# Kernel tuning notes

Measured on AMD Instinct MI355X. Metric: run time of the kernel, lower is better.

## Reference

```python
import jax, jax.numpy as jnp
import numpy as np

N_NODES = 100000
N_EDGES = 1600000
IN_CH = 128
HID = 128
NUM_CLASSES = 10
NUM_GRAPHS = 128
SLOPE = 0.01  # F.leaky_relu default negative_slope


def _lin_params(key, fan_in, fan_out):
    kw, kb = jax.random.split(key)
    bound = 1.0 / np.sqrt(fan_in)
    W = jax.random.uniform(kw, (fan_in, fan_out), jnp.float32, -bound, bound)
    b = jax.random.uniform(kb, (fan_out,), jnp.float32, -bound, bound)
    return W, b


def setup_inputs() -> dict:
    key = jax.random.key(0)
    ks = jax.random.split(key, 8)
    x = jax.random.normal(ks[0], (N_NODES, IN_CH), jnp.float32)
    edge_index = jax.random.randint(ks[1], (2, N_EDGES), 0, N_NODES, jnp.int64)
    batch = jnp.sort(jax.random.randint(ks[2], (N_NODES,), 0, NUM_GRAPHS, jnp.int64))
    W1, b1 = _lin_params(ks[3], IN_CH, HID)
    W2, b2 = _lin_params(ks[4], HID, HID)
    W3, b3 = _lin_params(ks[5], HID, HID // 2)
    W4, b4 = _lin_params(ks[6], HID // 2, HID // 2)
    W5, b5 = _lin_params(ks[7], HID // 2, NUM_CLASSES)
    return {"x": x, "edge_index": edge_index, "batch": batch,
            "W1": W1, "b1": b1, "W2": W2, "b2": b2,
            "W3": W3, "b3": b3, "W4": W4, "b4": b4, "W5": W5, "b5": b5}


def gcn_conv(x, src, dst, W, b):
    # PyG GCNConv: h = x W; add self-loops; symmetric norm D^-1/2 (A+I) D^-1/2
    h = x @ W  # [N, F]
    n = x.shape[0]
    deg = jnp.zeros((n,), h.dtype).at[dst].add(1.0) + 1.0  # includes self-loop
    dinv = jax.lax.rsqrt(deg)
    norm = dinv[src] * dinv[dst]  # [E]
    agg = jnp.zeros_like(h).at[dst].add(h[src] * norm[:, None])
    agg = agg + h * (dinv * dinv)[:, None]  # self-loop term: 1/deg
    return agg + b


def reference(x, edge_index, batch, W1, b1, W2, b2, W3, b3, W4, b4, W5, b5):
    src, dst = edge_index[0], edge_index[1]
    h = jax.nn.leaky_relu(gcn_conv(x, src, dst, W1, b1), SLOPE)
    h = jax.nn.leaky_relu(gcn_conv(h, src, dst, W2, b2), SLOPE)
    # global mean pool over graphs
    sums = jax.ops.segment_sum(h, batch, num_segments=NUM_GRAPHS)
    cnts = jax.ops.segment_sum(jnp.ones((h.shape[0],), h.dtype), batch,
                               num_segments=NUM_GRAPHS)
    g = sums / jnp.maximum(cnts, 1.0)[:, None]  # [NUM_GRAPHS, HID]
    g = jax.nn.leaky_relu(g @ W3 + b3, SLOPE)
    g = jax.nn.leaky_relu(g @ W4 + b4, SLOPE)
    return g @ W5 + b5
```

## Files before the change

### kernel.cpp

```cpp
#include <hip/hip_runtime.h>
#include <hip/hip_bf16.h>


#define SLOPE 0.01f

__device__ __forceinline__ float lrelu(float x) { return x > 0.f ? x : SLOPE * x; }

__device__ __forceinline__ unsigned short f2bf(float f) {
    union { float f; unsigned u; } v; v.f = f;
    unsigned r = v.u + 0x7fffu + ((v.u >> 16) & 1u);
    return (unsigned short)(r >> 16);
}
__device__ __forceinline__ float bf_lo(unsigned x) {
    union { unsigned u; float f; } v; v.u = x << 16; return v.f;
}
__device__ __forceinline__ float bf_hi(unsigned x) {
    union { unsigned u; float f; } v; v.u = x & 0xffff0000u; return v.f;
}
__device__ __forceinline__ unsigned packbf(float lo, float hi) {
    return (unsigned)f2bf(lo) | ((unsigned)f2bf(hi) << 16);
}

typedef __attribute__((ext_vector_type(8))) short bf16x8;
typedef __attribute__((ext_vector_type(4))) float f32x4;
typedef __attribute__((ext_vector_type(2))) float f32x2;

#define LDA 136
#define CAPP 5120
#define MAXBUCK 400

__global__ void k_init(int* __restrict__ zbase, int nz,
                       const float* __restrict__ W1, unsigned short* __restrict__ WT1,
                       const float* __restrict__ W2, unsigned short* __restrict__ WT2,
                       const int* __restrict__ batch, int* __restrict__ gstart,
                       int N, int NG) {
    int b = blockIdx.x;
    if (b < 64) {
        int idx = b * 256 + threadIdx.x;
        int k = idx >> 7, n = idx & 127;
        WT1[n * 128 + k] = f2bf(W1[idx]);
    } else if (b < 128) {
        int idx = (b - 64) * 256 + threadIdx.x;
        int k = idx >> 7, n = idx & 127;
        WT2[n * 128 + k] = f2bf(W2[idx]);
    } else if (b == 128) {
        int g = threadIdx.x;
        if (g <= NG) {
            int lo = 0, hi = N;
            while (lo < hi) { int mid = (lo + hi) >> 1; if (batch[mid] < g) lo = mid + 1; else hi = mid; }
            gstart[g] = lo;
        }
    } else {
        int i = (b - 129) * 256 + threadIdx.x;
        if (i < nz) zbase[i] = 0;
    }
}

template<bool IN_BF16, bool SCALE>
__device__ __forceinline__ void gemm_body(const void* __restrict__ Xv,
                                          const unsigned short* __restrict__ WT,
                                          unsigned short* __restrict__ Y, int M,
                                          unsigned short* Bs, int bid,
                                          const float* __restrict__ dinvg) {
    int t = threadIdx.x;
    int row0 = bid * 64;
    int w = t >> 6, l = t & 63;
    int lr = l & 15;
    int ko = (l >> 4) * 8;

    int gr = row0 + w * 16 + lr;
    bool inb = gr < M;
    bf16x8 afr[4];
    if (IN_BF16) {
        const unsigned short* Xrow = (const unsigned short*)Xv + (size_t)gr * 128;
#pragma unroll
        for (int kc = 0; kc < 4; ++kc) {
            if (inb) afr[kc] = *(const bf16x8*)&Xrow[kc * 32 + ko];
            else     afr[kc] = (bf16x8){0, 0, 0, 0, 0, 0, 0, 0};
        }
    } else {
        const float* Xrow = (const float*)Xv + (size_t)gr * 128;
#pragma unroll
        for (int kc = 0; kc < 4; ++kc) {
            if (inb) {
                float4 u0 = *(const float4*)&Xrow[kc * 32 + ko];
                float4 u1 = *(const float4*)&Xrow[kc * 32 + ko + 4];
                union { bf16x8 v; unsigned u[4]; } cv;
                cv.u[0] = packbf(u0.x, u0.y);
                cv.u[1] = packbf(u0.z, u0.w);
                cv.u[2] = packbf(u1.x, u1.y);
                cv.u[3] = packbf(u1.z, u1.w);
                afr[kc] = cv.v;
            } else afr[kc] = (bf16x8){0, 0, 0, 0, 0, 0, 0, 0};
        }
    }

    {
        const uint4* WT4 = (const uint4*)WT;
#pragma unroll
        for (int i = 0; i < 8; ++i) {
            int idx = t + i * 256;
            int n = idx >> 4, c8 = idx & 15;
            *(uint4*)&Bs[n * LDA + c8 * 8] = WT4[idx];
        }
    }
    __syncthreads();

    f32x4 acc[8];
#pragma unroll
    for (int c = 0; c < 8; ++c) acc[c] = (f32x4){0.f, 0.f, 0.f, 0.f};

#pragma unroll
    for (int kc = 0; kc < 4; ++kc) {
        int kb = kc * 32 + ko;
        bf16x8 bfr[8];
#pragma unroll
        for (int ct = 0; ct < 8; ++ct)
            bfr[ct] = *(const bf16x8*)&Bs[(ct * 16 + lr) * LDA + kb];
#pragma unroll
        for (int ct = 0; ct < 8; ++ct)
            acc[ct] = __builtin_amdgcn_mfma_f32_16x16x32_bf16(afr[kc], bfr[ct], acc[ct], 0, 0, 0);
    }

    __syncthreads();
    int qr = (l >> 4) * 4;
#pragma unroll
    for (int i = 0; i < 4; ++i) {
        int r = w * 16 + qr + i;
        float sc = 1.f;
        if (SCALE) {
            int gr2 = row0 + r;
            sc = (gr2 < M) ? dinvg[gr2] : 1.f;
        }
#pragma unroll
        for (int ct = 0; ct < 8; ++ct)
            Bs[r * LDA + ct * 16 + lr] = f2bf(acc[ct][i] * sc);
    }
    __syncthreads();
    {
        uint4* Y4 = (uint4*)Y;
#pragma unroll
        for (int i = 0; i < 4; ++i) {
            int idx = t + i * 256;
            int r = idx >> 4, c8 = idx & 15;
            int g2 = row0 + r;
            if (g2 < M) Y4[(size_t)g2 * 16 + c8] = *(const uint4*)&Bs[r * LDA + c8 * 8];
        }
    }
}

__device__ __forceinline__ void p1_body(const int* __restrict__ src,
                                        const int* __restrict__ dst,
                                        int E, int nb, int* __restrict__ g_cnt,
                                        unsigned* __restrict__ part,
                                        int* hist, int bid) {
    int* base = hist + MAXBUCK;
    int t = threadIdx.x;
    for (int b = t; b < nb; b += 256) hist[b] = 0;
    __syncthreads();
    int e0b = bid * 4096;
#pragma unroll
    for (int j = 0; j < 4; ++j) {
        int e = e0b + j * 1024 + t * 4;
        if (e + 3 < E) {
            int4 d = *(const int4*)&dst[e];
            atomicAdd(&hist[d.x >> 8], 1);
            atomicAdd(&hist[d.y >> 8], 1);
            atomicAdd(&hist[d.z >> 8], 1);
            atomicAdd(&hist[d.w >> 8], 1);
        } else {
            for (int k = e; k < E && k < e + 4; ++k)
                atomicAdd(&hist[dst[k] >> 8], 1);
        }
    }
    __syncthreads();
    for (int b = t; b < nb; b += 256) {
        int c = hist[b];
        base[b] = c ? atomicAdd(&g_cnt[b], c) : 0;
        hist[b] = 0;
    }
    __syncthreads();
#pragma unroll
    for (int j = 0; j < 4; ++j) {
        int e = e0b + j * 1024 + t * 4;
        if (e + 3 < E) {
            int4 d = *(const int4*)&dst[e];
            int4 s = *(const int4*)&src[e];
            int bk, p;
            bk = d.x >> 8; p = base[bk] + atomicAdd(&hist[bk], 1);
            if (p < CAPP) part[(size_t)bk * CAPP + p] = ((unsigned)s.x << 8) | ((unsigned)d.x & 255u);
            bk = d.y >> 8; p = base[bk] + atomicAdd(&hist[bk], 1);
            if (p < CAPP) part[(size_t)bk * CAPP + p] = ((unsigned)s.y << 8) | ((unsigned)d.y & 255u);
            bk = d.z >> 8; p = base[bk] + atomicAdd(&hist[bk], 1);
            if (p < CAPP) part[(size_t)bk * CAPP + p] = ((unsigned)s.z << 8) | ((unsigned)d.z & 255u);
            bk = d.w >> 8; p = base[bk] + atomicAdd(&hist[bk], 1);
            if (p < CAPP) part[(size_t)bk * CAPP + p] = ((unsigned)s.w << 8) | ((unsigned)d.w & 255u);
        } else {
            for (int k = e; k < E && k < e + 4; ++k) {
                int bk = dst[k] >> 8;
                int p = base[bk] + atomicAdd(&hist[bk], 1);
                if (p < CAPP) part[(size_t)bk * CAPP + p] = ((unsigned)src[k] << 8) | ((unsigned)dst[k] & 255u);
            }
        }
    }
}

__global__ __launch_bounds__(256) void k_p1_gemm1(
    const int* __restrict__ src, const int* __restrict__ dst, int E, int nb,
    int* __restrict__ g_cnt, unsigned* __restrict__ part, int nbP1,
    const float* __restrict__ X, const unsigned short* __restrict__ WT,
    unsigned short* __restrict__ Y, int M) {
    __shared__ __align__(16) unsigned short Bs[128 * LDA];
    int b = blockIdx.x;
    if (b < nbP1) p1_body(src, dst, E, nb, g_cnt, part, (int*)Bs, b);
    else gemm_body<false, false>((const void*)X, WT, Y, M, Bs, b - nbP1, nullptr);
}

__global__ __launch_bounds__(256) void k_p2(const unsigned* __restrict__ part,
                                            const int* __restrict__ g_cnt,
                                            int* __restrict__ csr,
                                            int2* __restrict__ rpz,
                                            float* __restrict__ dinvg,
                                            unsigned short* __restrict__ H, int N) {
    __shared__ int cnt[256];
    __shared__ int sc[256];
    __shared__ float dvl[256];
    int b = blockIdx.x, t = threadIdx.x;
    int nbase = b << 8;
    int nn = N - nbase; if (nn > 256) nn = 256;

    cnt[t] = 0;
    __syncthreads();

    int Eb = g_cnt[b]; if (Eb > CAPP) Eb = CAPP;
    const unsigned* pp = part + (size_t)b * CAPP;
    for (int i = t; i < Eb; i += 256)
        atomicAdd(&cnt[pp[i] & 255u], 1);
    __syncthreads();

    int v = cnt[t];
    sc[t] = v;
    __syncthreads();
    for (int off = 1; off < 256; off <<= 1) {
        int add = (t >= off) ? sc[t - off] : 0;
        __syncthreads();
        sc[t] += add;
        __syncthreads();
    }
    int excl = sc[t] - v;

    float di = rsqrtf((float)v + 1.0f);
    if (t < nn) {
        rpz[nbase + t] = make_int2(b * CAPP + excl, b * CAPP + excl + v);
        dinvg[nbase + t] = di;
    }
    dvl[t] = di;
    cnt[t] = excl;
    __syncthreads();

    for (int i = t; i < Eb; i += 256) {
        unsigned pv = pp[i];
        int lcl = pv & 255u;
        int p = atomicAdd(&cnt[lcl], 1);
        csr[(size_t)b * CAPP + p] = (int)(pv >> 8);
    }

    uint4* H4 = (uint4*)H;
    int tot = nn * 16;
    for (int i = t; i < tot; i += 256) {
        int r = i >> 4, c = i & 15;
        float d = dvl[r];
        uint4 hv = H4[(size_t)(nbase + r) * 16 + c];
        uint4 o;
        o.x = packbf(bf_lo(hv.x) * d, bf_hi(hv.x) * d);
        o.y = packbf(bf_lo(hv.y) * d, bf_hi(hv.y) * d);
        o.z = packbf(bf_lo(hv.z) * d, bf_hi(hv.z) * d);
        o.w = packbf(bf_lo(hv.w) * d, bf_hi(hv.w) * d);
        H4[(size_t)(nbase + r) * 16 + c] = o;
    }
}

__global__ __launch_bounds__(256) void k_gemm2(
    const void* __restrict__ Xv, const unsigned short* __restrict__ WT,
    unsigned short* __restrict__ Y, int M, const float* __restrict__ dinvg) {
    __shared__ __align__(16) unsigned short Bs[128 * LDA];
    gemm_body<true, true>(Xv, WT, Y, M, Bs, blockIdx.x, dinvg);
}

__device__ __forceinline__ void acc8(f32x2& S0, f32x2& S1, f32x2& S2, f32x2& S3,
                                     uint4 hv) {
    f32x2 t;
    t.x = bf_lo(hv.x); t.y = bf_hi(hv.x); S0 += t;
    t.x = bf_lo(hv.y); t.y = bf_hi(hv.y); S1 += t;
    t.x = bf_lo(hv.z); t.y = bf_hi(hv.z); S2 += t;
    t.x = bf_lo(hv.w); t.y = bf_hi(hv.w); S3 += t;
}

__device__ __forceinline__ void agg_node_f(const uint4* __restrict__ H4,
                                           const int* __restrict__ csr,
                                           int e0, int e1, int u, float du,
                                           const float* __restrict__ bias, int cl,
                                           float* __restrict__ a) {
    uint4 hs = H4[(size_t)u * 16 + cl];
    f32x2 A0 = {0.f, 0.f}, A1 = {0.f, 0.f}, A2 = {0.f, 0.f}, A3 = {0.f, 0.f};
    f32x2 B0 = {0.f, 0.f}, B1 = {0.f, 0.f}, B2 = {0.f, 0.f}, B3 = {0.f, 0.f};

    int e = e0;
    while (e < e1) {
        int nn = e1 - e; if (nn > 16) nn = 16;
        int ci = (cl < nn) ? csr[e + cl] : 0;
        int j = 0;
        for (; j + 4 <= nn; j += 4) {
            int i0 = __shfl(ci, j,     16);
            int i1 = __shfl(ci, j + 1, 16);
            int i2 = __shfl(ci, j + 2, 16);
            int i3 = __shfl(ci, j + 3, 16);
            uint4 hA = H4[(size_t)i0 * 16 + cl];
            uint4 hB = H4[(size_t)i1 * 16 + cl];
            uint4 hC = H4[(size_t)i2 * 16 + cl];
            uint4 hD = H4[(size_t)i3 * 16 + cl];
            acc8(A0, A1, A2, A3, hA);
            acc8(B0, B1, B2, B3, hB);
            acc8(A0, A1, A2, A3, hC);
            acc8(B0, B1, B2, B3, hD);
        }
        for (; j < nn; ++j) {
            int i0 = __shfl(ci, j, 16);
            uint4 hA = H4[(size_t)i0 * 16 + cl];
            acc8(A0, A1, A2, A3, hA);
        }
        e += nn;
    }

    acc8(A0, A1, A2, A3, hs);
    A0 += B0; A1 += B1; A2 += B2; A3 += B3;

    float4 c0 = *(const float4*)&bias[cl * 8];
    float4 c1 = *(const float4*)&bias[cl * 8 + 4];
    a[0] = lrelu(A0.x * du + c0.x); a[1] = lrelu(A0.y * du + c0.y);
    a[2] = lrelu(A1.x * du + c0.z); a[3] = lrelu(A1.y * du + c0.w);
    a[4] = lrelu(A2.x * du + c1.x); a[5] = lrelu(A2.y * du + c1.y);
    a[6] = lrelu(A3.x * du + c1.z); a[7] = lrelu(A3.y * du + c1.w);
}

__global__ __launch_bounds__(256) void k_agg7(const unsigned short* __restrict__ H,
                                              const int* __restrict__ csr,
                                              const int2* __restrict__ rpz,
                                              const float* __restrict__ dinvg,
                                              const float* __restrict__ bias,
                                              unsigned short* __restrict__ OUT, int N) {
    int t = threadIdx.x;
    int grp = t >> 4, cl = t & 15;
    int u = blockIdx.x * 16 + grp;
    if (u >= N) return;
    const uint4* H4 = (const uint4*)H;
    int2 rz = rpz[u];
    float du = dinvg[u];
    float a[8];
    agg_node_f(H4, csr, rz.x, rz.y, u, du, bias, cl, a);
    uint4 o;
    o.x = packbf(a[0], a[1]);
    o.y = packbf(a[2], a[3]);
    o.z = packbf(a[4], a[5]);
    o.w = packbf(a[6], a[7]);
    ((uint4*)OUT)[(size_t)u * 16 + cl] = o;
}

__global__ __launch_bounds__(256) void k_agg7p(const unsigned short* __restrict__ H,
                                               const int* __restrict__ csr,
                                               const int2* __restrict__ rpz,
                                               const float* __restrict__ dinvg,
                                               const float* __restrict__ bias,
                                               const int* __restrict__ batch,
                                               float* __restrict__ Gsum, int N) {
    __shared__ float P[16][132];
    __shared__ int gb[16];
    int t = threadIdx.x;
    int grp = t >> 4, cl = t & 15;
    int u = blockIdx.x * 16 + grp;
    if (blockIdx.x * 16 >= N) return;

    float a[8] = {0.f, 0.f, 0.f, 0.f, 0.f, 0.f, 0.f, 0.f};
    if (u < N) {
        const uint4* H4 = (const uint4*)H;
        int2 rz = rpz[u];
        float du = dinvg[u];
        agg_node_f(H4, csr, rz.x, rz.y, u, du, bias, cl, a);
    }
    if (cl == 0) gb[grp] = (u < N) ? batch[u] : -1;
#pragma unroll
    for (int j = 0; j < 8; ++j) P[grp][cl * 8 + j] = a[j];
    __syncthreads();

    if (t < 128) {
        float run = 0.f;
        int cur = -1;
        for (int i = 0; i < 16; ++i) {
            int g = gb[i];
            if (g < 0) break;
            if (g != cur) {
                if (cur >= 0) atomicAdd(&Gsum[cur * 128 + t], run);
                run = 0.f; cur = g;
            }
            run += P[i][t];
        }
        if (cur >= 0) atomicAdd(&Gsum[cur * 128 + t], run);
    }
}

__global__ __launch_bounds__(64) void k_mlp(const float* __restrict__ Gsum,
                                            const int* __restrict__ gstart,
                                            const float* __restrict__ W3, const float* __restrict__ b3,
                                            const float* __restrict__ W4, const float* __restrict__ b4,
                                            const float* __restrict__ W5, const float* __restrict__ b5,
                                            float* __restrict__ OUT) {
    __shared__ float row[128];
    __shared__ float t1[64];
    __shared__ float t2[64];
    int g = blockIdx.x, t = threadIdx.x;
    float inv = 1.0f / fmaxf((float)(gstart[g + 1] - gstart[g]), 1.0f);
    row[t]      = Gsum[g * 128 + t] * inv;
    row[t + 64] = Gsum[g * 128 + t + 64] * inv;
    __syncthreads();
    float acc = b3[t];
    for (int k = 0; k < 128; ++k) acc += row[k] * W3[k * 64 + t];
    t1[t] = lrelu(acc);
    __syncthreads();
    acc = b4[t];
    for (int k = 0; k < 64; ++k) acc += t1[k] * W4[k * 64 + t];
    t2[t] = lrelu(acc);
    __syncthreads();
    if (t < 10) {
        acc = b5[t];
        for (int k = 0; k < 64; ++k) acc += t2[k] * W5[k * 10 + t];
        OUT[g * 10 + t] = acc;
    }
}


extern "C" void kernel_launch(void* const* d_in, const int* in_sizes, int n_in,
                              void* d_out, int out_size, void* d_ws, size_t ws_size,
                              hipStream_t stream) {
    const float* x    = (const float*)d_in[0];
    const int*   ei   = (const int*)d_in[1];
    const int*   batch= (const int*)d_in[2];
    const float* W1   = (const float*)d_in[3];
    const float* b1   = (const float*)d_in[4];
    const float* W2   = (const float*)d_in[5];
    const float* b2   = (const float*)d_in[6];
    const float* W3   = (const float*)d_in[7];
    const float* b3   = (const float*)d_in[8];
    const float* W4   = (const float*)d_in[9];
    const float* b4   = (const float*)d_in[10];
    const float* W5   = (const float*)d_in[11];
    const float* b5   = (const float*)d_in[12];
    float* out = (float*)d_out;

    const int N = in_sizes[2];
    const int E = in_sizes[1] / 2;
    const int NG = 128;

    const int* src = ei;
    const int* dst = ei + E;

    char* w = (char*)d_ws;
    unsigned short* bufA = (unsigned short*)w; w += (size_t)N * 128 * 2;
    unsigned short* bufB = (unsigned short*)w; w += (size_t)N * 128 * 2;
    int*   g_cnt = (int*)w;   w += 512 * 4;
    float* gsum  = (float*)w; w += (size_t)NG * 128 * 4;
    int*   gstart= (int*)w;   w += 512 * 4;
    float* dinv  = (float*)w; w += (size_t)N * 4;
    int2*  rpz   = (int2*)w;  w += (size_t)N * 8;
    unsigned* part = (unsigned*)w; w += (size_t)MAXBUCK * CAPP * 4;
    int*   csr   = (int*)w;   w += (size_t)MAXBUCK * CAPP * 4;
    unsigned short* WT1 = (unsigned short*)w; w += 128 * 128 * 2;
    unsigned short* WT2 = (unsigned short*)w; w += 128 * 128 * 2;
    (void)ws_size; (void)n_in; (void)out_size;

    int nbB  = (N + 255) >> 8;
    int nbP1 = (E + 4095) / 4096;
    int nbG  = (N + 63) / 64;
    int nZero = 512 + NG * 128;
    int nbZ  = (nZero + 255) / 256;

    k_init<<<129 + nbZ, 256, 0, stream>>>(g_cnt, nZero, W1, WT1, W2, WT2,
                                          batch, gstart, N, NG);
    k_p1_gemm1<<<nbP1 + nbG, 256, 0, stream>>>(src, dst, E, nbB, g_cnt, part,
                                               nbP1, x, WT1, bufA, N);
    k_p2<<<nbB, 256, 0, stream>>>(part, g_cnt, csr, rpz, dinv, bufA, N);

    int nbA = (N + 15) / 16;

    k_agg7<<<nbA, 256, 0, stream>>>(bufA, csr, rpz, dinv, b1, bufB, N);
    k_gemm2<<<nbG, 256, 0, stream>>>(bufB, WT2, bufA, N, dinv);
    k_agg7p<<<nbA, 256, 0, stream>>>(bufA, csr, rpz, dinv, b2, batch, gsum, N);

    k_mlp<<<NG, 64, 0, stream>>>(gsum, gstart, W3, b3, W4, b4, W5, b5, out);
}
```

Baseline: 314.7 us.

## Fuse layer-1 aggregation with layer-2 GEMM into one kernel

Result: no change. 319.7 us (+1.6%).

```diff
diff --git a/kernel.cpp b/kernel.cpp
--- a/kernel.cpp
+++ b/kernel.cpp
@@ -280,13 +280,6 @@
     }
 }
 
-__global__ __launch_bounds__(256) void k_gemm2(
-    const void* __restrict__ Xv, const unsigned short* __restrict__ WT,
-    unsigned short* __restrict__ Y, int M, const float* __restrict__ dinvg) {
-    __shared__ __align__(16) unsigned short Bs[128 * LDA];
-    gemm_body<true, true>(Xv, WT, Y, M, Bs, blockIdx.x, dinvg);
-}
-
 __device__ __forceinline__ void acc8(f32x2& S0, f32x2& S1, f32x2& S2, f32x2& S3,
                                      uint4 hv) {
     f32x2 t;
@@ -343,27 +336,73 @@
     a[6] = lrelu(A3.x * du + c1.z); a[7] = lrelu(A3.y * du + c1.w);
 }
 
-__global__ __launch_bounds__(256) void k_agg7(const unsigned short* __restrict__ H,
-                                              const int* __restrict__ csr,
-                                              const int2* __restrict__ rpz,
-                                              const float* __restrict__ dinvg,
-                                              const float* __restrict__ bias,
-                                              unsigned short* __restrict__ OUT, int N) {
+__global__ __launch_bounds__(256) void k_aggemm2(
+    const unsigned short* __restrict__ H,
+    const int* __restrict__ csr, const int2* __restrict__ rpz,
+    const float* __restrict__ dinvg, const float* __restrict__ bias,
+    const unsigned short* __restrict__ WT,
+    unsigned short* __restrict__ Y, int N) {
+    __shared__ __align__(16) unsigned short As[16 * LDA];
     int t = threadIdx.x;
     int grp = t >> 4, cl = t & 15;
-    int u = blockIdx.x * 16 + grp;
-    if (u >= N) return;
-    const uint4* H4 = (const uint4*)H;
-    int2 rz = rpz[u];
-    float du = dinvg[u];
-    float a[8];
-    agg_node_f(H4, csr, rz.x, rz.y, u, du, bias, cl, a);
-    uint4 o;
-    o.x = packbf(a[0], a[1]);
-    o.y = packbf(a[2], a[3]);
-    o.z = packbf(a[4], a[5]);
-    o.w = packbf(a[6], a[7]);
-    ((uint4*)OUT)[(size_t)u * 16 + cl] = o;
+    int row0 = blockIdx.x * 16;
+    int u = row0 + grp;
+    if (row0 >= N) return;
+
+    float a[8] = {0.f, 0.f, 0.f, 0.f, 0.f, 0.f, 0.f, 0.f};
+    if (u < N) {
+        const uint4* H4 = (const uint4*)H;
+        int2 rz = rpz[u];
+        float du = dinvg[u];
+        agg_node_f(H4, csr, rz.x, rz.y, u, du, bias, cl, a);
+    }
+    {
+        uint4 o;
+        o.x = packbf(a[0], a[1]);
+        o.y = packbf(a[2], a[3]);
+        o.z = packbf(a[4], a[5]);
+        o.w = packbf(a[6], a[7]);
+        *(uint4*)&As[grp * LDA + cl * 8] = o;
+    }
+    __syncthreads();
+
+    int w = t >> 6, l = t & 63;
+    int lr = l & 15;
+    int ko = (l >> 4) * 8;
+
+    f32x4 acc[2];
+    acc[0] = (f32x4){0.f, 0.f, 0.f, 0.f};
+    acc[1] = (f32x4){0.f, 0.f, 0.f, 0.f};
+#pragma unroll
+    for (int kc = 0; kc < 4; ++kc) {
+        int kb = kc * 32 + ko;
+        bf16x8 afr = *(const bf16x8*)&As[lr * LDA + kb];
+#pragma unroll
+        for (int ct = 0; ct < 2; ++ct) {
+            int n = (w * 2 + ct) * 16 + lr;
+            bf16x8 bfr = *(const bf16x8*)&WT[(size_t)n * 128 + kb];
+            acc[ct] = __builtin_amdgcn_mfma_f32_16x16x32_bf16(afr, bfr, acc[ct], 0, 0, 0);
+        }
+    }
+
+    __syncthreads();
+    int qr = (l >> 4) * 4;
+#pragma unroll
+    for (int i = 0; i < 4; ++i) {
+        int r = qr + i;
+        int gu = row0 + r;
+        float sc = (gu < N) ? dinvg[gu] : 1.f;
+#pragma unroll
+        for (int ct = 0; ct < 2; ++ct)
+            As[r * LDA + (w * 2 + ct) * 16 + lr] = f2bf(acc[ct][i] * sc);
+    }
+    __syncthreads();
+    {
+        int r = t >> 4, c8 = t & 15;
+        int gu = row0 + r;
+        if (gu < N)
+            ((uint4*)Y)[(size_t)gu * 16 + c8] = *(const uint4*)&As[r * LDA + c8 * 8];
+    }
 }
 
 __global__ __launch_bounds__(256) void k_agg7p(const unsigned short* __restrict__ H,
@@ -491,9 +530,8 @@
 
     int nbA = (N + 15) / 16;
 
-    k_agg7<<<nbA, 256, 0, stream>>>(bufA, csr, rpz, dinv, b1, bufB, N);
-    k_gemm2<<<nbG, 256, 0, stream>>>(bufB, WT2, bufA, N, dinv);
-    k_agg7p<<<nbA, 256, 0, stream>>>(bufA, csr, rpz, dinv, b2, batch, gsum, N);
+    k_aggemm2<<<nbA, 256, 0, stream>>>(bufA, csr, rpz, dinv, b1, WT2, bufB, N);
+    k_agg7p<<<nbA, 256, 0, stream>>>(bufB, csr, rpz, dinv, b2, batch, gsum, N);
 
     k_mlp<<<NG, 64, 0, stream>>>(gsum, gstart, W3, b3, W4, b4, W5, b5, out);
 }
```
